# Optimization experiments

Measured on AMD Instinct MI355X. Metric: run time of the kernel, lower is better.

The kernel has to match this reference:

```python
import jax, jax.numpy as jnp
import numpy as np

B, T, D = 4, 2048, 1024
H, KD, VD = 16, 64, 64  # num_heads, key_dim, value_dim; H*KD == D


def setup_inputs() -> dict:
    key = jax.random.key(0)
    ks = jax.random.split(key, 10)
    s = 0.02
    return {
        "q_in": jax.random.normal(ks[0], (B, T, D), jnp.float32),
        "v_in": jax.random.normal(ks[1], (B, T, D), jnp.float32),
        "Wq": jax.random.normal(ks[2], (D, H * KD), jnp.float32) * s,
        "bq": jnp.zeros((H * KD,), jnp.float32),
        "Wk": jax.random.normal(ks[3], (D, H * KD), jnp.float32) * s,
        "bk": jnp.zeros((H * KD,), jnp.float32),
        "Wv": jax.random.normal(ks[4], (D, H * VD), jnp.float32) * s,
        "bv": jnp.zeros((H * VD,), jnp.float32),
        "Wo": jax.random.normal(ks[5], (H * VD, D), jnp.float32) * s,
        "bo": jnp.zeros((D,), jnp.float32),
    }


def reference(q_in, v_in, Wq, bq, Wk, bk, Wv, bv, Wo, bo):
    # QKV projections (key defaults to value input)
    q = q_in @ Wq + bq                      # [B,T,H*KD]
    k = v_in @ Wk + bk                      # [B,T,H*KD]
    v = v_in @ Wv + bv                      # [B,T,H*VD]
    q = q.reshape(B, T, H, KD)
    k = k.reshape(B, T, H, KD)
    v = v.reshape(B, T, H, VD)
    # scaled dot-product attention, scores materialized as [B,H,Tq,Tv]
    q = q / jnp.sqrt(jnp.asarray(KD, q.dtype))
    scores = jnp.einsum('bqnh,bvnh->bnqv', q, k)
    weights = jax.nn.softmax(scores, axis=-1)
    out = jnp.einsum('bnqv,bvnh->bqnh', weights, v)  # [B,Tq,H,VD]
    out = out.reshape(B, T, H * VD)
    return out @ Wo + bo                    # [B,T,D]
```

## Files before the change

### kernel.cpp

```cpp
#include <hip/hip_runtime.h>

#define BATCH  4
#define T_SEQ  2048
#define NH     16
#define DMODEL 1024
#define HD     64

typedef float    f32x4 __attribute__((ext_vector_type(4)));
typedef _Float16 f16x8 __attribute__((ext_vector_type(8)));
typedef _Float16 f16x4 __attribute__((ext_vector_type(4)));

#define LOG2E 1.44269504088896f

__device__ __forceinline__ void lds_load16(const void* g, void* l) {
  __builtin_amdgcn_global_load_lds((const __attribute__((address_space(1))) void*)g,
                                   (__attribute__((address_space(3))) void*)l, 16, 0, 0);
}

__global__ __launch_bounds__(256) void cast2_f32_to_f16(
    const float* __restrict__ a, const float* __restrict__ bsrc,
    _Float16* __restrict__ oa, _Float16* __restrict__ ob, int n4) {
  const float* in = blockIdx.y ? bsrc : a;
  _Float16* out = blockIdx.y ? ob : oa;
  int i = blockIdx.x * 256 + threadIdx.x;
  if (i < n4) {
    float4 v = ((const float4*)in)[i];
    f16x4 o = { (_Float16)v.x, (_Float16)v.y, (_Float16)v.z, (_Float16)v.w };
    ((f16x4*)out)[i] = o;
  }
}

__global__ __launch_bounds__(256) void transcast_w4(
    const float* __restrict__ W0, const float* __restrict__ W1,
    const float* __restrict__ W2, const float* __restrict__ W3,
    _Float16* __restrict__ T0, _Float16* __restrict__ T1,
    _Float16* __restrict__ T2, _Float16* __restrict__ T3) {
  const float* W; _Float16* Wt;
  switch (blockIdx.z) {
    case 0: W = W0; Wt = T0; break;
    case 1: W = W1; Wt = T1; break;
    case 2: W = W2; Wt = T2; break;
    default: W = W3; Wt = T3; break;
  }
  __shared__ float L[64][65];
  const int n0 = blockIdx.x * 64, k0 = blockIdx.y * 64;
  const int tx = threadIdx.x & 15, ty = threadIdx.x >> 4;
#pragma unroll
  for (int i = 0; i < 4; ++i) {
    float4 v = *(const float4*)&W[(size_t)(k0 + ty + 16 * i) * DMODEL + n0 + tx * 4];
    L[ty + 16 * i][tx * 4 + 0] = v.x;
    L[ty + 16 * i][tx * 4 + 1] = v.y;
    L[ty + 16 * i][tx * 4 + 2] = v.z;
    L[ty + 16 * i][tx * 4 + 3] = v.w;
  }
  __syncthreads();
#pragma unroll
  for (int i = 0; i < 4; ++i) {
    int n = n0 + ty + 16 * i;
    f16x4 o;
#pragma unroll
    for (int j = 0; j < 4; ++j) o[j] = (_Float16)L[tx * 4 + j][ty + 16 * i];
    *(f16x4*)&Wt[(size_t)n * DMODEL + k0 + tx * 4] = o;
  }
}

__global__ __launch_bounds__(256) void transpose_v(
    const _Float16* __restrict__ V, _Float16* __restrict__ Vt) {
  __shared__ _Float16 L[64][72];
  const int tid = threadIdx.x;
  const int b = blockIdx.z, h = blockIdx.y, t0 = blockIdx.x * 64;
#pragma unroll
  for (int i = 0; i < 2; ++i) {
    int r = (tid >> 3) + 32 * i, dc = (tid & 7) * 8;
    f16x8 v = *(const f16x8*)&V[(((size_t)b * T_SEQ + t0 + r) * NH + h) * HD + dc];
    *(f16x8*)&L[r][dc] = v;
  }
  __syncthreads();
#pragma unroll
  for (int i = 0; i < 2; ++i) {
    int d = tid & 63, tt = (tid >> 6) * 16 + i * 8;
    f16x8 o;
#pragma unroll
    for (int j = 0; j < 8; ++j) o[j] = L[tt + j][d];
    *(f16x8*)&Vt[(((size_t)b * NH + h) * HD + d) * T_SEQ + t0 + tt] = o;
  }
}

template <bool OUT32>
__device__ __forceinline__ void gemm_body(
    const _Float16* __restrict__ A, const _Float16* __restrict__ Wt,
    const float* __restrict__ bias, void* __restrict__ Cout, float scale,
    _Float16* As, _Float16* Bs) {
  const int K = DMODEL, N = DMODEL;
  const int tid = threadIdx.x, lane = tid & 63, wave = tid >> 6;
  const int bid = blockIdx.x + blockIdx.y * gridDim.x;
  const int m0 = ((bid & 7) * 8 + ((bid >> 3) & 7)) * 128;
  const int n0 = (bid >> 6) * 128;
  const int wm = (wave & 1) * 4, wn = (wave >> 1) * 4;
  const int m16 = lane & 15, quad = lane >> 4;

  const _Float16* ap[4]; const _Float16* bp[4];
  _Float16* da[4]; _Float16* db[4];
#pragma unroll
  for (int i = 0; i < 4; ++i) {
    int gi = wave * 4 + i;
    int row = (gi >> 1) * 16 + m16;
    int kof = (gi & 1) * 32 + quad * 8;
    ap[i] = A  + (size_t)(m0 + row) * K + kof;
    bp[i] = Wt + (size_t)(n0 + row) * K + kof;
    da[i] = As + gi * 512;
    db[i] = Bs + gi * 512;
  }

  f32x4 acc[4][4] = {};

#pragma unroll
  for (int k0 = 0; k0 < 1024; k0 += 64) {
    __syncthreads();
#pragma unroll
    for (int i = 0; i < 4; ++i) {
      lds_load16(ap[i] + k0, da[i]);
      lds_load16(bp[i] + k0, db[i]);
    }
    __syncthreads();
#pragma unroll
    for (int s = 0; s < 2; ++s) {
      f16x8 af[4], bf[4];
#pragma unroll
      for (int t = 0; t < 4; ++t) {
        af[t] = *(const f16x8*)(As + (((wm + t) * 2 + s) * 64 + lane) * 8);
        bf[t] = *(const f16x8*)(Bs + (((wn + t) * 2 + s) * 64 + lane) * 8);
      }
#pragma unroll
      for (int mi = 0; mi < 4; ++mi)
#pragma unroll
        for (int ni = 0; ni < 4; ++ni)
          acc[mi][ni] = __builtin_amdgcn_mfma_f32_16x16x32_f16(af[mi], bf[ni], acc[mi][ni], 0, 0, 0);
    }
  }

#pragma unroll
  for (int mi = 0; mi < 4; ++mi)
#pragma unroll
    for (int r = 0; r < 4; ++r) {
      int row = m0 + (wm + mi) * 16 + quad * 4 + r;
#pragma unroll
      for (int ni = 0; ni < 4; ++ni) {
        int col = n0 + (wn + ni) * 16 + m16;
        float v = (acc[mi][ni][r] + bias[col]) * scale;
        if (OUT32) ((float*)Cout)[(size_t)row * N + col] = v;
        else       ((_Float16*)Cout)[(size_t)row * N + col] = (_Float16)v;
      }
    }
}

__global__ __launch_bounds__(256) void gemm_qkv(
    const _Float16* __restrict__ Aq, const _Float16* __restrict__ Av,
    const _Float16* __restrict__ Wq, const _Float16* __restrict__ Wk,
    const _Float16* __restrict__ Wv,
    const float* __restrict__ bq, const float* __restrict__ bk,
    const float* __restrict__ bv,
    _Float16* __restrict__ Cq, _Float16* __restrict__ Ck, _Float16* __restrict__ Cv) {
  __shared__ _Float16 As[128 * 64];
  __shared__ _Float16 Bs[128 * 64];
  const _Float16* A; const _Float16* Wt; const float* bias; _Float16* C; float scale;
  if (blockIdx.z == 0)      { A = Aq; Wt = Wq; bias = bq; C = Cq; scale = 0.125f * LOG2E; }
  else if (blockIdx.z == 1) { A = Av; Wt = Wk; bias = bk; C = Ck; scale = 1.f; }
  else                      { A = Av; Wt = Wv; bias = bv; C = Cv; scale = 1.f; }
  gemm_body<false>(A, Wt, bias, C, scale, As, Bs);
}

__global__ __launch_bounds__(256) void gemm_out(
    const _Float16* __restrict__ A, const _Float16* __restrict__ Wt,
    const float* __restrict__ bias, float* __restrict__ Cout) {
  __shared__ _Float16 As[128 * 64];
  __shared__ _Float16 Bs[128 * 64];
  gemm_body<true>(A, Wt, bias, Cout, 1.f, As, Bs);
}

__global__ __launch_bounds__(256) void attn_mfma(
    const _Float16* __restrict__ Q, const _Float16* __restrict__ Kb,
    const _Float16* __restrict__ Vt, _Float16* __restrict__ O) {
  __shared__ _Float16 Ks[64 * 64];
  __shared__ _Float16 Vs[64 * 64];
  __shared__ _Float16 Ps[4 * 2048];

  const int tid = threadIdx.x, lane = tid & 63, wave = tid >> 6;
  const int m16 = lane & 15, quad = lane >> 4;
  const int bidl = blockIdx.x + 16 * blockIdx.y + 256 * blockIdx.z;
  const int h = bidl & 15;
  const int q0 = ((bidl >> 4) & 15) * 128;
  const int b = bidl >> 8;
  const int wq = wave * 32;
  const int wbase = wave * 2048;

  f16x8 qf[2][2];
#pragma unroll
  for (int mi = 0; mi < 2; ++mi)
#pragma unroll
    for (int ki = 0; ki < 2; ++ki) {
      int q = q0 + wq + mi * 16 + m16;
      qf[mi][ki] = *(const f16x8*)(Q + (((size_t)b * T_SEQ + q) * NH + h) * HD + ki * 32 + quad * 8);
    }

  const _Float16 *kp[2], *vp[2];
  _Float16 *dk[2], *dvp[2];
#pragma unroll
  for (int i = 0; i < 2; ++i) {
    int g = wave * 128 + i * 64 + lane;
    int tk = (g >> 7) * 16 + (g & 15);
    int dkof = ((g >> 6) & 1) * 32 + ((g >> 4) & 3) * 8;
    kp[i] = Kb + (((size_t)b * T_SEQ + tk) * NH + h) * HD + dkof;
    int dvof = (g >> 7) * 16 + (g & 15);
    int tv = ((g >> 6) & 1) * 32 + ((g >> 4) & 3) * 8;
    vp[i] = Vt + (((size_t)b * NH + h) * HD + dvof) * T_SEQ + tv;
    dk[i]  = Ks + (wave * 2 + i) * 512;
    dvp[i] = Vs + (wave * 2 + i) * 512;
  }

  int pw[2][4];
#pragma unroll
  for (int mi = 0; mi < 2; ++mi)
#pragma unroll
    for (int nt = 0; nt < 4; ++nt) {
      int kt = nt >> 1;
      int q8 = ((nt & 1) << 1) | (quad >> 1);
      pw[mi][nt] = wbase + ((mi * 2 + kt) * 64 + q8 * 16 + m16) * 8 + (quad & 1) * 4;
    }

  const f16x8 onef = {(_Float16)1, (_Float16)1, (_Float16)1, (_Float16)1,
                      (_Float16)1, (_Float16)1, (_Float16)1, (_Float16)1};

  f32x4 o_acc[2][4] = {};
  f32x4 l_acc[2] = {};

  for (int kv = 0; kv < T_SEQ; kv += 64) {
    __syncthreads();
    lds_load16(kp[0], dk[0]);
    lds_load16(kp[1], dk[1]);
    lds_load16(vp[0], dvp[0]);
    lds_load16(vp[1], dvp[1]);
    kp[0] += 64 * NH * HD; kp[1] += 64 * NH * HD;
    vp[0] += 64; vp[1] += 64;
    __syncthreads();

    f32x4 st[2][4] = {};
#pragma unroll
    for (int nt = 0; nt < 4; ++nt)
#pragma unroll
      for (int ki = 0; ki < 2; ++ki) {
        f16x8 kf = *(const f16x8*)(Ks + ((nt * 2 + ki) * 64 + lane) * 8);
        st[0][nt] = __builtin_amdgcn_mfma_f32_16x16x32_f16(kf, qf[0][ki], st[0][nt], 0, 0, 0);
        st[1][nt] = __builtin_amdgcn_mfma_f32_16x16x32_f16(kf, qf[1][ki], st[1][nt], 0, 0, 0);
      }

#pragma unroll
    for (int mi = 0; mi < 2; ++mi)
#pragma unroll
      for (int nt = 0; nt < 4; ++nt) {
        f16x4 p;
#pragma unroll
        for (int r = 0; r < 4; ++r)
          p[r] = (_Float16)__builtin_amdgcn_exp2f(st[mi][nt][r]);
        *(f16x4*)(Ps + pw[mi][nt]) = p;
      }

#pragma unroll
    for (int kt = 0; kt < 2; ++kt) {
      f16x8 pf0 = *(const f16x8*)(Ps + wbase + ((0 * 2 + kt) * 64 + lane) * 8);
      f16x8 pf1 = *(const f16x8*)(Ps + wbase + ((1 * 2 + kt) * 64 + lane) * 8);
      l_acc[0] = __builtin_amdgcn_mfma_f32_16x16x32_f16(pf0, onef, l_acc[0], 0, 0, 0);
      l_acc[1] = __builtin_amdgcn_mfma_f32_16x16x32_f16(pf1, onef, l_acc[1], 0, 0, 0);
#pragma unroll
      for (int nd = 0; nd < 4; ++nd) {
        f16x8 vf = *(const f16x8*)(Vs + ((nd * 2 + kt) * 64 + lane) * 8);
        o_acc[0][nd] = __builtin_amdgcn_mfma_f32_16x16x32_f16(pf0, vf, o_acc[0][nd], 0, 0, 0);
        o_acc[1][nd] = __builtin_amdgcn_mfma_f32_16x16x32_f16(pf1, vf, o_acc[1][nd], 0, 0, 0);
      }
    }
  }

#pragma unroll
  for (int mi = 0; mi < 2; ++mi)
#pragma unroll
    for (int r = 0; r < 4; ++r) {
      float inv = 1.f / l_acc[mi][r];
      int q = q0 + wq + mi * 16 + quad * 4 + r;
#pragma unroll
      for (int nd = 0; nd < 4; ++nd) {
        int d = nd * 16 + m16;
        O[(((size_t)b * T_SEQ + q) * NH + h) * HD + d] = (_Float16)(o_acc[mi][nd][r] * inv);
      }
    }
}

extern "C" void kernel_launch(void* const* d_in, const int* in_sizes, int n_in,
                              void* d_out, int out_size, void* d_ws, size_t ws_size,
                              hipStream_t stream) {
  const float* q_in = (const float*)d_in[0];
  const float* v_in = (const float*)d_in[1];
  const float* Wq   = (const float*)d_in[2];
  const float* bq   = (const float*)d_in[3];
  const float* Wk   = (const float*)d_in[4];
  const float* bk   = (const float*)d_in[5];
  const float* Wv   = (const float*)d_in[6];
  const float* bv   = (const float*)d_in[7];
  const float* Wo   = (const float*)d_in[8];
  const float* bo   = (const float*)d_in[9];
  float* out = (float*)d_out;

  const size_t MB = 1u << 20;
  char* ws = (char*)d_ws;
  _Float16* q16  = (_Float16*)(ws);
  _Float16* v16  = (_Float16*)(ws + 16 * MB);
  _Float16* qbuf = (_Float16*)(ws + 32 * MB);
  _Float16* kbuf = (_Float16*)(ws + 48 * MB);
  _Float16* vbuf = (_Float16*)(ws + 64 * MB);
  _Float16* Wqt  = (_Float16*)(ws + 80 * MB);
  _Float16* Wkt  = (_Float16*)(ws + 82 * MB);
  _Float16* Wvt  = (_Float16*)(ws + 84 * MB);
  _Float16* Wot  = (_Float16*)(ws + 86 * MB);

  const int n4 = BATCH * T_SEQ * DMODEL / 4;
  cast2_f32_to_f16<<<dim3(n4 / 256, 2), 256, 0, stream>>>(q_in, v_in, q16, v16, n4);

  transcast_w4<<<dim3(16, 16, 4), 256, 0, stream>>>(Wq, Wk, Wv, Wo, Wqt, Wkt, Wvt, Wot);

  dim3 gg(DMODEL / 128, BATCH * T_SEQ / 128, 3);
  gemm_qkv<<<gg, 256, 0, stream>>>(q16, v16, Wqt, Wkt, Wvt, bq, bk, bv, qbuf, kbuf, vbuf);

  _Float16* Vt = q16;
  transpose_v<<<dim3(32, 16, 4), 256, 0, stream>>>(vbuf, Vt);

  attn_mfma<<<dim3(16, 16, 4), 256, 0, stream>>>(qbuf, kbuf, Vt, qbuf);

  gemm_out<<<dim3(8, 64), 256, 0, stream>>>(qbuf, Wot, bo, out);
}
```

Before: 372.4 us.

## Double-buffer LDS tiles in GEMMs and attention, fuse V transpose into QKV GEMM

Adds two-stage LDS double buffering to the projection GEMMs and the attention K/V loop, so the next tile's global-to-LDS load is issued before computing on the current one. This replaces two barriers per iteration with one. The V projection epilogue now writes V directly in transposed [B,H,D,T] layout, which removes the separate transpose kernel and its round trip through memory. Softmax probabilities are packed with cvt_pkrtz, which rounds toward zero and can shift numerics slightly. LDS usage doubles, which may lower occupancy.

```diff
diff --git a/kernel.cpp b/kernel.cpp
--- a/kernel.cpp
+++ b/kernel.cpp
@@ -9,12 +9,20 @@
 typedef float    f32x4 __attribute__((ext_vector_type(4)));
 typedef _Float16 f16x8 __attribute__((ext_vector_type(8)));
 typedef _Float16 f16x4 __attribute__((ext_vector_type(4)));
+typedef __fp16   h16x2 __attribute__((ext_vector_type(2)));
 
 #define LOG2E 1.44269504088896f
 
 __device__ __forceinline__ void lds_load16(const void* g, void* l) {
   __builtin_amdgcn_global_load_lds((const __attribute__((address_space(1))) void*)g,
                                    (__attribute__((address_space(3))) void*)l, 16, 0, 0);
+}
+
+__device__ __forceinline__ f16x4 pack4_f16(float a, float b, float c, float d) {
+  union { h16x2 h[2]; f16x4 f; } u;
+  u.h[0] = __builtin_amdgcn_cvt_pkrtz(a, b);
+  u.h[1] = __builtin_amdgcn_cvt_pkrtz(c, d);
+  return u.f;
 }
 
 __global__ __launch_bounds__(256) void cast2_f32_to_f16(
@@ -64,33 +72,10 @@
   }
 }
 
-__global__ __launch_bounds__(256) void transpose_v(
-    const _Float16* __restrict__ V, _Float16* __restrict__ Vt) {
-  __shared__ _Float16 L[64][72];
-  const int tid = threadIdx.x;
-  const int b = blockIdx.z, h = blockIdx.y, t0 = blockIdx.x * 64;
-#pragma unroll
-  for (int i = 0; i < 2; ++i) {
-    int r = (tid >> 3) + 32 * i, dc = (tid & 7) * 8;
-    f16x8 v = *(const f16x8*)&V[(((size_t)b * T_SEQ + t0 + r) * NH + h) * HD + dc];
-    *(f16x8*)&L[r][dc] = v;
-  }
-  __syncthreads();
-#pragma unroll
-  for (int i = 0; i < 2; ++i) {
-    int d = tid & 63, tt = (tid >> 6) * 16 + i * 8;
-    f16x8 o;
-#pragma unroll
-    for (int j = 0; j < 8; ++j) o[j] = L[tt + j][d];
-    *(f16x8*)&Vt[(((size_t)b * NH + h) * HD + d) * T_SEQ + t0 + tt] = o;
-  }
-}
-
-template <bool OUT32>
 __device__ __forceinline__ void gemm_body(
     const _Float16* __restrict__ A, const _Float16* __restrict__ Wt,
     const float* __restrict__ bias, void* __restrict__ Cout, float scale,
-    _Float16* As, _Float16* Bs) {
+    int mode, _Float16* As0, _Float16* Bs0, _Float16* As1, _Float16* Bs1) {
   const int K = DMODEL, N = DMODEL;
   const int tid = threadIdx.x, lane = tid & 63, wave = tid >> 6;
   const int bid = blockIdx.x + blockIdx.y * gridDim.x;
@@ -100,7 +85,6 @@
   const int m16 = lane & 15, quad = lane >> 4;
 
   const _Float16* ap[4]; const _Float16* bp[4];
-  _Float16* da[4]; _Float16* db[4];
 #pragma unroll
   for (int i = 0; i < 4; ++i) {
     int gi = wave * 4 + i;
@@ -108,28 +92,25 @@
     int kof = (gi & 1) * 32 + quad * 8;
     ap[i] = A  + (size_t)(m0 + row) * K + kof;
     bp[i] = Wt + (size_t)(n0 + row) * K + kof;
-    da[i] = As + gi * 512;
-    db[i] = Bs + gi * 512;
   }
 
   f32x4 acc[4][4] = {};
 
-#pragma unroll
-  for (int k0 = 0; k0 < 1024; k0 += 64) {
-    __syncthreads();
+  auto stage = [&](int k0, _Float16* Asb, _Float16* Bsb) {
 #pragma unroll
     for (int i = 0; i < 4; ++i) {
-      lds_load16(ap[i] + k0, da[i]);
-      lds_load16(bp[i] + k0, db[i]);
-    }
-    __syncthreads();
+      lds_load16(ap[i] + k0, Asb + (wave * 4 + i) * 512);
+      lds_load16(bp[i] + k0, Bsb + (wave * 4 + i) * 512);
+    }
+  };
+  auto compute = [&](const _Float16* Asb, const _Float16* Bsb) {
 #pragma unroll
     for (int s = 0; s < 2; ++s) {
       f16x8 af[4], bf[4];
 #pragma unroll
       for (int t = 0; t < 4; ++t) {
-        af[t] = *(const f16x8*)(As + (((wm + t) * 2 + s) * 64 + lane) * 8);
-        bf[t] = *(const f16x8*)(Bs + (((wn + t) * 2 + s) * 64 + lane) * 8);
+        af[t] = *(const f16x8*)(Asb + (((wm + t) * 2 + s) * 64 + lane) * 8);
+        bf[t] = *(const f16x8*)(Bsb + (((wn + t) * 2 + s) * 64 + lane) * 8);
       }
 #pragma unroll
       for (int mi = 0; mi < 4; ++mi)
@@ -137,21 +118,49 @@
         for (int ni = 0; ni < 4; ++ni)
           acc[mi][ni] = __builtin_amdgcn_mfma_f32_16x16x32_f16(af[mi], bf[ni], acc[mi][ni], 0, 0, 0);
     }
-  }
-
-#pragma unroll
-  for (int mi = 0; mi < 4; ++mi)
-#pragma unroll
-    for (int r = 0; r < 4; ++r) {
-      int row = m0 + (wm + mi) * 16 + quad * 4 + r;
+  };
+
+  stage(0, As0, Bs0);
+  __syncthreads();
+#pragma unroll
+  for (int k0 = 0; k0 < 1024; k0 += 128) {
+    stage(k0 + 64, As1, Bs1);
+    compute(As0, Bs0);
+    __syncthreads();
+    if (k0 + 128 < 1024) stage(k0 + 128, As0, Bs0);
+    compute(As1, Bs1);
+    __syncthreads();
+  }
+
+  if (mode == 2) {
+#pragma unroll
+    for (int mi = 0; mi < 4; ++mi)
 #pragma unroll
       for (int ni = 0; ni < 4; ++ni) {
+        int row = m0 + (wm + mi) * 16 + quad * 4;
         int col = n0 + (wn + ni) * 16 + m16;
-        float v = (acc[mi][ni][r] + bias[col]) * scale;
-        if (OUT32) ((float*)Cout)[(size_t)row * N + col] = v;
-        else       ((_Float16*)Cout)[(size_t)row * N + col] = (_Float16)v;
-      }
-    }
+        int bb = row >> 11, tt = row & (T_SEQ - 1);
+        int hh = col >> 6, dd = col & 63;
+        float bv = bias[col];
+        f16x4 pv = pack4_f16(acc[mi][ni][0] + bv, acc[mi][ni][1] + bv,
+                             acc[mi][ni][2] + bv, acc[mi][ni][3] + bv);
+        *(f16x4*)&((_Float16*)Cout)[(((size_t)bb * NH + hh) * HD + dd) * T_SEQ + tt] = pv;
+      }
+  } else {
+#pragma unroll
+    for (int mi = 0; mi < 4; ++mi)
+#pragma unroll
+      for (int r = 0; r < 4; ++r) {
+        int row = m0 + (wm + mi) * 16 + quad * 4 + r;
+#pragma unroll
+        for (int ni = 0; ni < 4; ++ni) {
+          int col = n0 + (wn + ni) * 16 + m16;
+          float v = (acc[mi][ni][r] + bias[col]) * scale;
+          if (mode == 1) ((float*)Cout)[(size_t)row * N + col] = v;
+          else           ((_Float16*)Cout)[(size_t)row * N + col] = (_Float16)v;
+        }
+      }
+  }
 }
 
 __global__ __launch_bounds__(256) void gemm_qkv(
@@ -161,28 +170,26 @@
     const float* __restrict__ bq, const float* __restrict__ bk,
     const float* __restrict__ bv,
     _Float16* __restrict__ Cq, _Float16* __restrict__ Ck, _Float16* __restrict__ Cv) {
-  __shared__ _Float16 As[128 * 64];
-  __shared__ _Float16 Bs[128 * 64];
-  const _Float16* A; const _Float16* Wt; const float* bias; _Float16* C; float scale;
-  if (blockIdx.z == 0)      { A = Aq; Wt = Wq; bias = bq; C = Cq; scale = 0.125f * LOG2E; }
-  else if (blockIdx.z == 1) { A = Av; Wt = Wk; bias = bk; C = Ck; scale = 1.f; }
-  else                      { A = Av; Wt = Wv; bias = bv; C = Cv; scale = 1.f; }
-  gemm_body<false>(A, Wt, bias, C, scale, As, Bs);
+  __shared__ _Float16 As0[128 * 64], Bs0[128 * 64], As1[128 * 64], Bs1[128 * 64];
+  const _Float16* A; const _Float16* Wt; const float* bias; _Float16* C;
+  float scale; int mode;
+  if (blockIdx.z == 0)      { A = Aq; Wt = Wq; bias = bq; C = Cq; scale = 0.125f * LOG2E; mode = 0; }
+  else if (blockIdx.z == 1) { A = Av; Wt = Wk; bias = bk; C = Ck; scale = 1.f; mode = 0; }
+  else                      { A = Av; Wt = Wv; bias = bv; C = Cv; scale = 1.f; mode = 2; }
+  gemm_body(A, Wt, bias, C, scale, mode, As0, Bs0, As1, Bs1);
 }
 
 __global__ __launch_bounds__(256) void gemm_out(
     const _Float16* __restrict__ A, const _Float16* __restrict__ Wt,
     const float* __restrict__ bias, float* __restrict__ Cout) {
-  __shared__ _Float16 As[128 * 64];
-  __shared__ _Float16 Bs[128 * 64];
-  gemm_body<true>(A, Wt, bias, Cout, 1.f, As, Bs);
+  __shared__ _Float16 As0[128 * 64], Bs0[128 * 64], As1[128 * 64], Bs1[128 * 64];
+  gemm_body(A, Wt, bias, Cout, 1.f, 1, As0, Bs0, As1, Bs1);
 }
 
 __global__ __launch_bounds__(256) void attn_mfma(
     const _Float16* __restrict__ Q, const _Float16* __restrict__ Kb,
     const _Float16* __restrict__ Vt, _Float16* __restrict__ O) {
-  __shared__ _Float16 Ks[64 * 64];
-  __shared__ _Float16 Vs[64 * 64];
+  __shared__ _Float16 Ks0[64 * 64], Vs0[64 * 64], Ks1[64 * 64], Vs1[64 * 64];
   __shared__ _Float16 Ps[4 * 2048];
 
   const int tid = threadIdx.x, lane = tid & 63, wave = tid >> 6;
@@ -204,7 +211,6 @@
     }
 
   const _Float16 *kp[2], *vp[2];
-  _Float16 *dk[2], *dvp[2];
 #pragma unroll
   for (int i = 0; i < 2; ++i) {
     int g = wave * 128 + i * 64 + lane;
@@ -214,8 +220,6 @@
     int dvof = (g >> 7) * 16 + (g & 15);
     int tv = ((g >> 6) & 1) * 32 + ((g >> 4) & 3) * 8;
     vp[i] = Vt + (((size_t)b * NH + h) * HD + dvof) * T_SEQ + tv;
-    dk[i]  = Ks + (wave * 2 + i) * 512;
-    dvp[i] = Vs + (wave * 2 + i) * 512;
   }
 
   int pw[2][4];
@@ -234,37 +238,34 @@
   f32x4 o_acc[2][4] = {};
   f32x4 l_acc[2] = {};
 
-  for (int kv = 0; kv < T_SEQ; kv += 64) {
-    __syncthreads();
-    lds_load16(kp[0], dk[0]);
-    lds_load16(kp[1], dk[1]);
-    lds_load16(vp[0], dvp[0]);
-    lds_load16(vp[1], dvp[1]);
-    kp[0] += 64 * NH * HD; kp[1] += 64 * NH * HD;
-    vp[0] += 64; vp[1] += 64;
-    __syncthreads();
-
+  auto stageKV = [&](int kv, _Float16* Kd, _Float16* Vd) {
+#pragma unroll
+    for (int i = 0; i < 2; ++i) {
+      lds_load16(kp[i] + (size_t)kv * (NH * HD), Kd + (wave * 2 + i) * 512);
+      lds_load16(vp[i] + kv, Vd + (wave * 2 + i) * 512);
+    }
+  };
+
+  auto tile = [&](const _Float16* Kd, const _Float16* Vd) {
     f32x4 st[2][4] = {};
 #pragma unroll
     for (int nt = 0; nt < 4; ++nt)
 #pragma unroll
       for (int ki = 0; ki < 2; ++ki) {
-        f16x8 kf = *(const f16x8*)(Ks + ((nt * 2 + ki) * 64 + lane) * 8);
+        f16x8 kf = *(const f16x8*)(Kd + ((nt * 2 + ki) * 64 + lane) * 8);
         st[0][nt] = __builtin_amdgcn_mfma_f32_16x16x32_f16(kf, qf[0][ki], st[0][nt], 0, 0, 0);
         st[1][nt] = __builtin_amdgcn_mfma_f32_16x16x32_f16(kf, qf[1][ki], st[1][nt], 0, 0, 0);
       }
-
 #pragma unroll
     for (int mi = 0; mi < 2; ++mi)
 #pragma unroll
       for (int nt = 0; nt < 4; ++nt) {
-        f16x4 p;
-#pragma unroll
-        for (int r = 0; r < 4; ++r)
-          p[r] = (_Float16)__builtin_amdgcn_exp2f(st[mi][nt][r]);
+        f16x4 p = pack4_f16(__builtin_amdgcn_exp2f(st[mi][nt][0]),
+                            __builtin_amdgcn_exp2f(st[mi][nt][1]),
+                            __builtin_amdgcn_exp2f(st[mi][nt][2]),
+                            __builtin_amdgcn_exp2f(st[mi][nt][3]));
         *(f16x4*)(Ps + pw[mi][nt]) = p;
       }
-
 #pragma unroll
     for (int kt = 0; kt < 2; ++kt) {
       f16x8 pf0 = *(const f16x8*)(Ps + wbase + ((0 * 2 + kt) * 64 + lane) * 8);
@@ -273,11 +274,22 @@
       l_acc[1] = __builtin_amdgcn_mfma_f32_16x16x32_f16(pf1, onef, l_acc[1], 0, 0, 0);
 #pragma unroll
       for (int nd = 0; nd < 4; ++nd) {
-        f16x8 vf = *(const f16x8*)(Vs + ((nd * 2 + kt) * 64 + lane) * 8);
+        f16x8 vf = *(const f16x8*)(Vd + ((nd * 2 + kt) * 64 + lane) * 8);
         o_acc[0][nd] = __builtin_amdgcn_mfma_f32_16x16x32_f16(pf0, vf, o_acc[0][nd], 0, 0, 0);
         o_acc[1][nd] = __builtin_amdgcn_mfma_f32_16x16x32_f16(pf1, vf, o_acc[1][nd], 0, 0, 0);
       }
     }
+  };
+
+  stageKV(0, Ks0, Vs0);
+  __syncthreads();
+  for (int kv = 0; kv < T_SEQ; kv += 128) {
+    stageKV(kv + 64, Ks1, Vs1);
+    tile(Ks0, Vs0);
+    __syncthreads();
+    if (kv + 128 < T_SEQ) stageKV(kv + 128, Ks0, Vs0);
+    tile(Ks1, Vs1);
+    __syncthreads();
   }
 
 #pragma unroll
@@ -315,7 +327,7 @@
   _Float16* v16  = (_Float16*)(ws + 16 * MB);
   _Float16* qbuf = (_Float16*)(ws + 32 * MB);
   _Float16* kbuf = (_Float16*)(ws + 48 * MB);
-  _Float16* vbuf = (_Float16*)(ws + 64 * MB);
+  _Float16* vtb  = (_Float16*)(ws + 64 * MB);
   _Float16* Wqt  = (_Float16*)(ws + 80 * MB);
   _Float16* Wkt  = (_Float16*)(ws + 82 * MB);
   _Float16* Wvt  = (_Float16*)(ws + 84 * MB);
@@ -327,12 +339,9 @@
   transcast_w4<<<dim3(16, 16, 4), 256, 0, stream>>>(Wq, Wk, Wv, Wo, Wqt, Wkt, Wvt, Wot);
 
   dim3 gg(DMODEL / 128, BATCH * T_SEQ / 128, 3);
-  gemm_qkv<<<gg, 256, 0, stream>>>(q16, v16, Wqt, Wkt, Wvt, bq, bk, bv, qbuf, kbuf, vbuf);
-
-  _Float16* Vt = q16;
-  transpose_v<<<dim3(32, 16, 4), 256, 0, stream>>>(vbuf, Vt);
-
-  attn_mfma<<<dim3(16, 16, 4), 256, 0, stream>>>(qbuf, kbuf, Vt, qbuf);
+  gemm_qkv<<<gg, 256, 0, stream>>>(q16, v16, Wqt, Wkt, Wvt, bq, bk, bv, qbuf, kbuf, vtb);
+
+  attn_mfma<<<dim3(16, 16, 4), 256, 0, stream>>>(qbuf, kbuf, vtb, qbuf);
 
   gemm_out<<<dim3(8, 64), 256, 0, stream>>>(qbuf, Wot, bo, out);
 }
```

Measured after the change: 359.3 us. -3.5%, faster.
